# Kernel tuning notes

Measured on AMD Instinct MI355X. Metric: run time of the kernel, lower is better.

The kernel has to match this reference:

```python
import jax, jax.numpy as jnp
import numpy as np

# irreps multiplicities
MUL0_N, MUL1_N = 64, 32   # node:   64x0e + 32x1o  -> dim 160
MUL0_E, MUL1_E = 8, 8     # edge:    8x0e +  8x1o  -> dim 32
MUL0_H, MUL1_H = 64, 32   # hidden: 64x0e + 32x1o  -> dim 160
N_NODES, N_EDGES = 50000, 800000
D_NODE = MUL0_N + 3 * MUL1_N
D_EDGE = MUL0_E + 3 * MUL1_E
D_HID = MUL0_H + 3 * MUL1_H


def _split(x, mul0, mul1):
    # split flat irreps feature into scalars [.., mul0] and vectors [.., mul1, 3]
    s = x[..., :mul0]
    v = x[..., mul0:].reshape(x.shape[0], mul1, 3)
    return s, v


def fctp_messages(x, e, W1, W2, W3, W4):
    """FullyConnectedTensorProduct(node_irreps, edge_irreps -> hidden_irreps), l<=1.
    Paths: (0e,0e->0e), (1o,1o->0e: delta/sqrt3), (0e,1o->1o), (1o,0e->1o)."""
    xs, xv = _split(x, MUL0_N, MUL1_N)   # [E,64], [E,32,3]
    es, ev = _split(e, MUL0_E, MUL1_E)   # [E,8],  [E,8,3]
    inv_sqrt2 = 1.0 / np.sqrt(2.0)       # 2 paths per output irrep
    s1 = jnp.einsum('ea,eb,abc->ec', xs, es, W1) * (1.0 / np.sqrt(MUL0_N * MUL0_E))
    s2 = jnp.einsum('eai,ebi,abc->ec', xv, ev, W2) * (1.0 / (np.sqrt(3.0) * np.sqrt(MUL1_N * MUL1_E)))
    out_s = (s1 + s2) * inv_sqrt2                         # [E,64]
    v1 = jnp.einsum('ea,ebi,abc->eci', xs, ev, W3) * (1.0 / np.sqrt(MUL0_N * MUL1_E))
    v2 = jnp.einsum('eai,eb,abc->eci', xv, es, W4) * (1.0 / np.sqrt(MUL1_N * MUL0_E))
    out_v = (v1 + v2) * inv_sqrt2                         # [E,32,3]
    return jnp.concatenate([out_s, out_v.reshape(out_v.shape[0], -1)], axis=-1)  # [E,160]


def setup_inputs() -> dict:
    key = jax.random.key(0)
    ks = jax.random.split(key, 12)
    node_features = jax.random.normal(ks[0], (N_NODES, D_NODE), dtype=jnp.float32)
    edge_index = jax.random.randint(ks[1], (2, N_EDGES), 0, N_NODES, dtype=jnp.int64)
    edge_attr_tensor = jax.random.normal(ks[2], (N_EDGES, D_EDGE), dtype=jnp.float32)
    node_attr_scalar_raw = jax.random.normal(ks[3], (N_NODES, 1), dtype=jnp.float32)
    # FCTP path weights (mul_in1, mul_in2, mul_out)
    W1 = jax.random.normal(ks[4], (MUL0_N, MUL0_E, MUL0_H), dtype=jnp.float32)
    W2 = jax.random.normal(ks[5], (MUL1_N, MUL1_E, MUL0_H), dtype=jnp.float32)
    W3 = jax.random.normal(ks[6], (MUL0_N, MUL1_E, MUL1_H), dtype=jnp.float32)
    W4 = jax.random.normal(ks[7], (MUL1_N, MUL0_E, MUL1_H), dtype=jnp.float32)
    # runtime-fallback dense layers (Gate raises at runtime in the original)
    Wm = jax.random.normal(ks[8], (D_HID, D_HID), dtype=jnp.float32) / np.sqrt(D_HID)
    bm = jnp.zeros((D_HID,), dtype=jnp.float32)
    Wu = jax.random.normal(ks[9], (D_NODE + D_HID, D_NODE), dtype=jnp.float32) / np.sqrt(D_NODE + D_HID)
    bu = jnp.zeros((D_NODE,), dtype=jnp.float32)
    return {"node_features": node_features, "edge_index": edge_index,
            "edge_attr_tensor": edge_attr_tensor, "node_attr_scalar_raw": node_attr_scalar_raw,
            "W1": W1, "W2": W2, "W3": W3, "W4": W4,
            "Wm": Wm, "bm": bm, "Wu": Wu, "bu": bu}


def reference(node_features, edge_index, edge_attr_tensor, node_attr_scalar_raw,
              W1, W2, W3, W4, Wm, bm, Wu, bu):
    row, col = edge_index[0], edge_index[1]
    # gather source nodes + equivariant tensor-product message
    tp = fctp_messages(node_features[col], edge_attr_tensor, W1, W2, W3, W4)  # [E,160]
    messages = tp @ Wm + bm                                                   # [E,160]
    # scatter-sum aggregation to destination nodes
    agg = jax.ops.segment_sum(messages, row, num_segments=N_NODES)            # [N,160]
    # update (runtime fallback: linear on concat) + residual
    upd = jnp.concatenate([node_features, agg], axis=-1) @ Wu + bu            # [N,160]
    return node_features + upd
```

## Files before the change

kernel.cpp:

```cpp
#include <hip/hip_runtime.h>
#include <hip/hip_bf16.h>

#define NN 50000
#define NE 800000
#define DN 160
#define DE 32
#define NP 50176

typedef __attribute__((ext_vector_type(2))) _Float16 f16x2;
typedef __attribute__((ext_vector_type(8))) _Float16 f16x8;
typedef __attribute__((ext_vector_type(4))) float f32x4;
typedef __attribute__((ext_vector_type(4))) unsigned short u16x4;

#define R2 0.81649658092772603f
#define R4 1.41421356237309515f
#define SC (1.0f/32.0f)

#define XST 172
#define EST 38

union AF { f16x2 p[4]; f16x8 v; };

__device__ __forceinline__ unsigned short f16bits(float f) {
    union { _Float16 h; unsigned short s; } u;
    u.h = (_Float16)f;
    return u.s;
}

__global__ __launch_bounds__(256) void xprep_kernel(const float* __restrict__ x,
                                                    unsigned short* __restrict__ xb) {
    int i = blockIdx.x * 256 + threadIdx.x;
    if (i < NN * DN / 4) {
        const float4 v = reinterpret_cast<const float4*>(x)[i];
        u16x4 p; p[0] = f16bits(v.x); p[1] = f16bits(v.y); p[2] = f16bits(v.z); p[3] = f16bits(v.w);
        reinterpret_cast<u16x4*>(xb)[i] = p;
    }
}

__global__ __launch_bounds__(256) void zero_kernel(float* __restrict__ T,
                                                   int* __restrict__ cnt) {
    int i = blockIdx.x * 256 + threadIdx.x;
    if (i < NN * DN) T[i] = 0.0f;
    if (i < NP) cnt[i] = 0;
}

__global__ __launch_bounds__(256) void hist_kernel(const int* __restrict__ eidx,
                                                   int* __restrict__ cnt) {
    int e = blockIdx.x * 256 + threadIdx.x;
    if (e < NE) atomicAdd(&cnt[eidx[e]], 1);
}

__global__ __launch_bounds__(256) void scan1_kernel(const int* __restrict__ cnt,
                                                    int* __restrict__ cursor,
                                                    int* __restrict__ bsum) {
    __shared__ int s[256];
    const int t = threadIdx.x;
    const int i = blockIdx.x * 256 + t;
    const int v = cnt[i];
    s[t] = v; __syncthreads();
    for (int off = 1; off < 256; off <<= 1) {
        int u = (t >= off) ? s[t - off] : 0;
        __syncthreads(); s[t] += u; __syncthreads();
    }
    cursor[i] = s[t] - v;
    if (t == 255) bsum[blockIdx.x] = s[255];
}

__global__ __launch_bounds__(256) void scan2_kernel(int* __restrict__ bsum) {
    __shared__ int s[256];
    const int t = threadIdx.x;
    const int v = (t < 196) ? bsum[t] : 0;
    s[t] = v; __syncthreads();
    for (int off = 1; off < 256; off <<= 1) {
        int u = (t >= off) ? s[t - off] : 0;
        __syncthreads(); s[t] += u; __syncthreads();
    }
    if (t < 196) bsum[t] = s[t] - v;
}

__global__ __launch_bounds__(256) void scan3_kernel(int* __restrict__ cursor,
                                                    const int* __restrict__ bsum) {
    int i = blockIdx.x * 256 + threadIdx.x;
    cursor[i] += bsum[blockIdx.x];
}

__global__ __launch_bounds__(256) void scatter_kernel(const int* __restrict__ eidx,
                                                      int* __restrict__ cursor,
                                                      int* __restrict__ sorted) {
    int e = blockIdx.x * 256 + threadIdx.x;
    if (e < NE) {
        int pos = atomicAdd(&cursor[eidx[e]], 1);
        sorted[pos] = e;
    }
}

__global__ __launch_bounds__(256) void wprep_edge_kernel(
    const float* __restrict__ W1, const float* __restrict__ W2,
    const float* __restrict__ W3, const float* __restrict__ W4,
    unsigned short* __restrict__ Wh)
{
    int id = blockIdx.x * 256 + threadIdx.x;
    if (id >= 73728) return;
    int j = id & 7, l = (id >> 3) & 63, st = id >> 9;
    int tt = st / 6, s = st % 6;
    int k = 32 * tt + 8 * (l >> 4) + j;
    float w;
    if (s < 4) {
        int c = s * 16 + (l & 15);
        if (k < 512) { int a = k >> 3, b = k & 7; w = W1[(a*8+b)*64 + c] * SC; }
        else { int k2 = k - 512; int a = k2 >> 3, b = k2 & 7; w = W2[(a*8+b)*64 + c] * (R2*SC); }
    } else {
        int c = (s - 4) * 16 + (l & 15);
        if (k < 512) { int a = k >> 3, b = k & 7; w = W3[(a*8+b)*32 + c] * SC; }
        else { int k2 = k - 512; int a = k2 >> 3, b = k2 & 7; w = W4[(a*8+b)*32 + c] * (R4*SC); }
    }
    Wh[id] = f16bits(w);
}

__global__ __launch_bounds__(256) void wcomp_kernel(
    const float* __restrict__ Wm, const float* __restrict__ bm,
    const float* __restrict__ Wu, float* __restrict__ Wc, float* __restrict__ bc)
{
    int id = blockIdx.x * 256 + threadIdx.x;
    if (id < 160 * 160) {
        int k = id / 160, c = id % 160;
        float s = 0.0f;
        for (int h = 0; h < 160; ++h) s = fmaf(Wm[k*160 + h], Wu[(160 + h)*160 + c], s);
        Wc[id] = s;
    }
    if (id < 160) {
        float s = 0.0f;
        for (int h = 0; h < 160; ++h) s = fmaf(bm[h], Wu[(160 + h)*160 + id], s);
        bc[id] = s;
    }
}

__global__ __launch_bounds__(256) void wprep_node_kernel(
    const float* __restrict__ Wu, const float* __restrict__ Wc,
    unsigned short* __restrict__ Wn)
{
    int id = blockIdx.x * 256 + threadIdx.x;
    if (id >= 51200) return;
    int j = id & 7, l = (id >> 3) & 63, tn = id >> 9;
    int tk = tn % 10, n16 = tn / 10;
    int c = n16 * 16 + (l & 15);
    int k = 32 * tk + 8 * (l >> 4) + j;
    float w;
    if (k < 160) {
        w = Wu[k * 160 + c];
    } else {
        int tcol = k - 160;
        int orig = (tcol < 64) ? tcol : 64 + ((tcol - 64) & 31) * 3 + ((tcol - 64) >> 5);
        w = Wc[orig * 160 + c];
    }
    Wn[id] = f16bits(w);
}

__device__ __forceinline__ void makeA(int tt, int g, int er,
    const unsigned short* __restrict__ xls,
    const f16x2 es2[4], const f16x2 ev2[3][4],
    AF& aS, AF& aV0, AF& aV1, AF& aV2)
{
    if (tt < 16) {
        const _Float16 xa = *reinterpret_cast<const _Float16*>(&xls[er*XST + 4*tt + g]);
        const f16x2 xa2 = (f16x2){xa, xa};
        #pragma unroll
        for (int p = 0; p < 4; ++p) {
            aS.p[p]  = xa2 * es2[p];
            aV0.p[p] = xa2 * ev2[0][p];
            aV1.p[p] = xa2 * ev2[1][p];
            aV2.p[p] = xa2 * ev2[2][p];
        }
    } else {
        const int a = 4 * (tt - 16) + g;
        const _Float16 x0 = *reinterpret_cast<const _Float16*>(&xls[er*XST + 64 + a*3 + 0]);
        const _Float16 x1 = *reinterpret_cast<const _Float16*>(&xls[er*XST + 64 + a*3 + 1]);
        const _Float16 x2 = *reinterpret_cast<const _Float16*>(&xls[er*XST + 64 + a*3 + 2]);
        const f16x2 x02 = (f16x2){x0, x0};
        const f16x2 x12 = (f16x2){x1, x1};
        const f16x2 x22 = (f16x2){x2, x2};
        #pragma unroll
        for (int p = 0; p < 4; ++p) {
            f16x2 d = x02 * ev2[0][p];
            d += x12 * ev2[1][p];
            d += x22 * ev2[2][p];
            aS.p[p]  = d;
            aV0.p[p] = x02 * es2[p];
            aV1.p[p] = x12 * es2[p];
            aV2.p[p] = x22 * es2[p];
        }
    }
}

template<int UXB>
__global__ __launch_bounds__(256, 3) void edge_kernel(
    const float* __restrict__ x, const unsigned short* __restrict__ xb,
    const int* __restrict__ eidx, const float* __restrict__ ea,
    const unsigned short* __restrict__ Wh,
    const int* __restrict__ sorted, float* __restrict__ T)
{
    __shared__ __align__(16) char smem[64*XST*2 + 64*EST*2];
    __shared__ int rowls[64];
    __shared__ int colls[64];
    __shared__ int sels[64];

    unsigned short* xls = (unsigned short*)smem;
    unsigned short* els = (unsigned short*)(smem + 64*XST*2);

    const int t = threadIdx.x;
    const int base = blockIdx.x * 64;

    if (t < 64) {
        const int se = sorted[base + t];
        sels[t] = se;
        rowls[t] = eidx[se];
        colls[t] = eidx[NE + se];
    }
    __syncthreads();

    if (UXB) {
        for (int j = t; j < 64 * 40; j += 256) {
            int m = j / 40, q = j - m * 40;
            const u16x4 v = *reinterpret_cast<const u16x4*>(xb + (size_t)colls[m] * DN + q * 4);
            *reinterpret_cast<u16x4*>(&xls[m*XST + q*4]) = v;
        }
    } else {
        for (int j = t; j < 64 * 40; j += 256) {
            int m = j / 40, q = j - m * 40;
            const float4 v = *reinterpret_cast<const float4*>(x + (size_t)colls[m] * DN + q * 4);
            u16x4 p; p[0] = f16bits(v.x); p[1] = f16bits(v.y); p[2] = f16bits(v.z); p[3] = f16bits(v.w);
            *reinterpret_cast<u16x4*>(&xls[m*XST + q*4]) = p;
        }
    }
    for (int j = t; j < 64 * 8; j += 256) {
        int m = j >> 3, q = j & 7;
        const float4 v = *reinterpret_cast<const float4*>(ea + (size_t)sels[m] * DE + q * 4);
        #pragma unroll
        for (int z = 0; z < 4; ++z) {
            int p = q * 4 + z;
            float val = (z == 0) ? v.x : (z == 1) ? v.y : (z == 2) ? v.z : v.w;
            int dst = (p < 8) ? p : 8 + ((p - 8) % 3) * 8 + (p - 8) / 3;
            els[m*EST + dst] = f16bits(val);
        }
    }
    __syncthreads();

    const int lane = t & 63;
    const int wv = t >> 6;
    const int r = lane & 15;
    const int g = lane >> 4;
    const int er = wv * 16 + r;

    f16x2 es2[4], ev2[3][4];
    #pragma unroll
    for (int p = 0; p < 4; ++p) {
        es2[p] = *reinterpret_cast<const f16x2*>(&els[er*EST + 2*p]);
        #pragma unroll
        for (int i = 0; i < 3; ++i)
            ev2[i][p] = *reinterpret_cast<const f16x2*>(&els[er*EST + 8 + i*8 + 2*p]);
    }

    f32x4 accS[4], accV[3][2];
    #pragma unroll
    for (int n = 0; n < 4; ++n) accS[n] = (f32x4){0.f, 0.f, 0.f, 0.f};
    #pragma unroll
    for (int i = 0; i < 3; ++i)
        #pragma unroll
        for (int n = 0; n < 2; ++n) accV[i][n] = (f32x4){0.f, 0.f, 0.f, 0.f};

    const unsigned short* wp = Wh + (size_t)lane * 8;

    f16x8 B0[6], B1[6];
    #pragma unroll
    for (int n = 0; n < 6; ++n)
        B0[n] = *reinterpret_cast<const f16x8*>(wp + n * 512);
    wp += 3072;

#define EDGE_MFMAS(B)                                                             \
    do {                                                                          \
        accS[0] = __builtin_amdgcn_mfma_f32_16x16x32_f16(aS.v,  B[0], accS[0],0,0,0); \
        accS[1] = __builtin_amdgcn_mfma_f32_16x16x32_f16(aS.v,  B[1], accS[1],0,0,0); \
        accS[2] = __builtin_amdgcn_mfma_f32_16x16x32_f16(aS.v,  B[2], accS[2],0,0,0); \
        accS[3] = __builtin_amdgcn_mfma_f32_16x16x32_f16(aS.v,  B[3], accS[3],0,0,0); \
        accV[0][0] = __builtin_amdgcn_mfma_f32_16x16x32_f16(aV0.v, B[4], accV[0][0],0,0,0); \
        accV[0][1] = __builtin_amdgcn_mfma_f32_16x16x32_f16(aV0.v, B[5], accV[0][1],0,0,0); \
        accV[1][0] = __builtin_amdgcn_mfma_f32_16x16x32_f16(aV1.v, B[4], accV[1][0],0,0,0); \
        accV[1][1] = __builtin_amdgcn_mfma_f32_16x16x32_f16(aV1.v, B[5], accV[1][1],0,0,0); \
        accV[2][0] = __builtin_amdgcn_mfma_f32_16x16x32_f16(aV2.v, B[4], accV[2][0],0,0,0); \
        accV[2][1] = __builtin_amdgcn_mfma_f32_16x16x32_f16(aV2.v, B[5], accV[2][1],0,0,0); \
    } while (0)

    for (int tt = 0; tt < 24; tt += 2) {
        #pragma unroll
        for (int n = 0; n < 6; ++n)
            B1[n] = *reinterpret_cast<const f16x8*>(wp + n * 512);
        wp += 3072;

        {
            AF aS, aV0, aV1, aV2;
            makeA(tt, g, er, xls, es2, ev2, aS, aV0, aV1, aV2);
            EDGE_MFMAS(B0);
        }

        if (tt + 2 < 24) {
            #pragma unroll
            for (int n = 0; n < 6; ++n)
                B0[n] = *reinterpret_cast<const f16x8*>(wp + n * 512);
            wp += 3072;
        }

        {
            AF aS, aV0, aV1, aV2;
            makeA(tt + 1, g, er, xls, es2, ev2, aS, aV0, aV1, aV2);
            EDGE_MFMAS(B1);
        }
    }
#undef EDGE_MFMAS

    __syncthreads();
    float* accw = (float*)smem;

    #pragma unroll
    for (int half = 0; half < 2; ++half) {
        if ((wv >> 1) == half) {
            const int lbase = (wv & 1) * 16 + g * 4;
            #pragma unroll
            for (int reg = 0; reg < 4; ++reg) {
                const int lrow = lbase + reg;
                #pragma unroll
                for (int n = 0; n < 4; ++n)
                    accw[lrow*161 + n*16 + r] = accS[n][reg];
                #pragma unroll
                for (int i = 0; i < 3; ++i)
                    #pragma unroll
                    for (int n = 0; n < 2; ++n)
                        accw[lrow*161 + 64 + i*32 + n*16 + r] = accV[i][n][reg];
            }
        }
        __syncthreads();

        if (t < DN) {
            const int col = t;
            const int ebase = half * 32;
            float s = 0.0f;
            int rstart = 0;
            for (int e = 0; e < 32; ++e) {
                s += accw[e*161 + col];
                const int ge = ebase + e;
                if (e == 31 || rowls[ge] != rowls[ge + 1]) {
                    float* dst = T + (size_t)rowls[ge] * DN + col;
                    if (rstart == 0 || e == 31) atomicAdd(dst, s);
                    else *dst = s;
                    s = 0.0f; rstart = e + 1;
                }
            }
        }
        __syncthreads();
    }
}

template<int UXB>
__global__ __launch_bounds__(256) void node_kernel(
    const float* __restrict__ x, const unsigned short* __restrict__ xb,
    float* __restrict__ T, const int* __restrict__ cnt,
    const unsigned short* __restrict__ Wn,
    const float* __restrict__ bu, const float* __restrict__ bc)
{
    __shared__ __align__(16) unsigned short A[64][328];
    const int t = threadIdx.x;
    const int nb = blockIdx.x * 64;

    if (UXB) {
        for (int j = t; j < 64 * 40; j += 256) {
            int m = j / 40, q = j - m * 40;
            int row = nb + m; if (row >= NN) row = NN - 1;
            const u16x4 v = *reinterpret_cast<const u16x4*>(xb + (size_t)row * DN + q * 4);
            *reinterpret_cast<u16x4*>(&A[m][q*4]) = v;
        }
    } else {
        for (int j = t; j < 64 * 40; j += 256) {
            int m = j / 40, q = j - m * 40;
            int row = nb + m; if (row >= NN) row = NN - 1;
            const float4 v = *reinterpret_cast<const float4*>(x + (size_t)row * DN + q * 4);
            u16x4 p; p[0] = f16bits(v.x); p[1] = f16bits(v.y); p[2] = f16bits(v.z); p[3] = f16bits(v.w);
            *reinterpret_cast<u16x4*>(&A[m][q*4]) = p;
        }
    }
    for (int j = t; j < 64 * 40; j += 256) {
        int m = j / 40, q = j - m * 40;
        int row = nb + m; if (row >= NN) row = NN - 1;
        const float4 v = *reinterpret_cast<const float4*>(T + (size_t)row * DN + q * 4);
        u16x4 p; p[0] = f16bits(v.x); p[1] = f16bits(v.y); p[2] = f16bits(v.z); p[3] = f16bits(v.w);
        *reinterpret_cast<u16x4*>(&A[m][160 + q*4]) = p;
    }
    __syncthreads();

    const int lane = t & 63;
    const int wv = t >> 6;
    const int r = lane & 15, g = lane >> 4;
    const int er = wv * 16 + r;

    f32x4 acc[10];
    #pragma unroll
    for (int n = 0; n < 10; ++n) acc[n] = (f32x4){0.f, 0.f, 0.f, 0.f};

    for (int tk = 0; tk < 10; ++tk) {
        const f16x8 a = *reinterpret_cast<const f16x8*>(&A[er][32 * tk + 8 * g]);
        #pragma unroll
        for (int n = 0; n < 10; ++n) {
            const f16x8 b = *reinterpret_cast<const f16x8*>(Wn + ((size_t)(n * 10 + tk) * 64 + lane) * 8);
            acc[n] = __builtin_amdgcn_mfma_f32_16x16x32_f16(a, b, acc[n], 0, 0, 0);
        }
    }

    #pragma unroll
    for (int reg = 0; reg < 4; ++reg) {
        const int nrow = nb + wv * 16 + g * 4 + reg;
        if (nrow < NN) {
            const float dg = (float)cnt[nrow];
            #pragma unroll
            for (int n = 0; n < 10; ++n) {
                const int c = n * 16 + r;
                T[(size_t)nrow * DN + c] =
                    acc[n][reg] + x[(size_t)nrow * DN + c] + bu[c] + dg * bc[c];
            }
        }
    }
}

extern "C" void kernel_launch(void* const* d_in, const int* in_sizes, int n_in,
                              void* d_out, int out_size, void* d_ws, size_t ws_size,
                              hipStream_t stream) {
    const float* xf   = (const float*)d_in[0];
    const int*   eidx = (const int*)d_in[1];
    const float* ea   = (const float*)d_in[2];
    const float* W1 = (const float*)d_in[4];
    const float* W2 = (const float*)d_in[5];
    const float* W3 = (const float*)d_in[6];
    const float* W4 = (const float*)d_in[7];
    const float* Wm = (const float*)d_in[8];
    const float* bm = (const float*)d_in[9];
    const float* Wu = (const float*)d_in[10];
    const float* bu = (const float*)d_in[11];

    float* out = (float*)d_out;

    char* ws = (char*)d_ws;
    int*            cnt    = (int*)ws;
    int*            cursor = (int*)(ws + (256 << 10));
    int*            sorted = (int*)(ws + (512 << 10));
    int*            bsum   = (int*)(ws + (3968 << 10));
    unsigned short* Wh     = (unsigned short*)(ws + (4096 << 10));
    float*          Wc     = (float*)(ws + (4352 << 10));
    float*          bc     = (float*)(ws + (4480 << 10));
    unsigned short* Wn     = (unsigned short*)(ws + (4608 << 10));
    unsigned short* xb     = (unsigned short*)(ws + (4864 << 10));

    const bool uxb = ws_size >= ((size_t)(4864 + 16000) << 10);

    wcomp_kernel<<<100, 256, 0, stream>>>(Wm, bm, Wu, Wc, bc);
    wprep_node_kernel<<<200, 256, 0, stream>>>(Wu, Wc, Wn);
    wprep_edge_kernel<<<288, 256, 0, stream>>>(W1, W2, W3, W4, Wh);
    if (uxb) xprep_kernel<<<(NN * DN / 4 + 255) / 256, 256, 0, stream>>>(xf, xb);
    zero_kernel<<<(NN * DN + 255) / 256, 256, 0, stream>>>(out, cnt);
    hist_kernel<<<NE / 256, 256, 0, stream>>>(eidx, cnt);
    scan1_kernel<<<NP / 256, 256, 0, stream>>>(cnt, cursor, bsum);
    scan2_kernel<<<1, 256, 0, stream>>>(bsum);
    scan3_kernel<<<NP / 256, 256, 0, stream>>>(cursor, bsum);
    scatter_kernel<<<NE / 256, 256, 0, stream>>>(eidx, cursor, sorted);
    if (uxb) {
        edge_kernel<1><<<NE / 64, 256, 0, stream>>>(xf, xb, eidx, ea, Wh, sorted, out);
        node_kernel<1><<<(NN + 63) / 64, 256, 0, stream>>>(xf, xb, out, cnt, Wn, bu, bc);
    } else {
        edge_kernel<0><<<NE / 64, 256, 0, stream>>>(xf, xb, eidx, ea, Wh, sorted, out);
        node_kernel<0><<<(NN + 63) / 64, 256, 0, stream>>>(xf, xb, out, cnt, Wn, bu, bc);
    }
}
```

Before: 517.9 us.

## Stage edge-kernel weight tiles through LDS with async global_load_lds double buffering

Replaces per-wave register double-buffered global loads of the packed weight matrix with a cooperative block-wide copy into a two-slot LDS buffer using global_load_lds. Each of the 24 k-steps then reads its B fragments from LDS, behind a barrier per step. The aim is to cut redundant global/L2 traffic, since every wave used to load the full weight tile itself, and to free registers. In exchange it adds 24 block barriers and extra LDS use (12 KB), which may lower occupancy. It also relies on the async LDS loads completing before the barrier, which only holds if the compiler inserts a vmcnt wait there.

New measurement: 469.5 us. 9.3% less time.

```diff
diff --git a/kernel.cpp b/kernel.cpp
--- a/kernel.cpp
+++ b/kernel.cpp
@@ -25,6 +25,12 @@
     union { _Float16 h; unsigned short s; } u;
     u.h = (_Float16)f;
     return u.s;
+}
+
+__device__ __forceinline__ void load_lds16(const void* g, void* l) {
+    __builtin_amdgcn_global_load_lds(
+        (const __attribute__((address_space(1))) unsigned int*)g,
+        (__attribute__((address_space(3))) unsigned int*)l, 16, 0, 0);
 }
 
 __global__ __launch_bounds__(256) void xprep_kernel(const float* __restrict__ x,
@@ -199,13 +205,14 @@
     const unsigned short* __restrict__ Wh,
     const int* __restrict__ sorted, float* __restrict__ T)
 {
-    __shared__ __align__(16) char smem[64*XST*2 + 64*EST*2];
+    __shared__ __align__(16) char smem[64*XST*2 + 64*EST*2 + 2*3072*2];
     __shared__ int rowls[64];
     __shared__ int colls[64];
     __shared__ int sels[64];
 
-    unsigned short* xls = (unsigned short*)smem;
-    unsigned short* els = (unsigned short*)(smem + 64*XST*2);
+    unsigned short* xls  = (unsigned short*)smem;
+    unsigned short* els  = (unsigned short*)(smem + 64*XST*2);
+    unsigned short* wbuf = (unsigned short*)(smem + 64*XST*2 + 64*EST*2);
 
     const int t = threadIdx.x;
     const int base = blockIdx.x * 64;
@@ -243,7 +250,6 @@
             els[m*EST + dst] = f16bits(val);
         }
     }
-    __syncthreads();
 
     const int lane = t & 63;
     const int wv = t >> 6;
@@ -251,6 +257,19 @@
     const int g = lane >> 4;
     const int er = wv * 16 + r;
 
+    #define STAGE_W(buf, tt)                                                       \
+        do {                                                                       \
+            const unsigned short* wsrc = Wh + (size_t)(tt) * 3072;                 \
+            unsigned short* wdst = wbuf + (buf) * 3072;                            \
+            load_lds16(wsrc + wv * 512 + lane * 8, wdst + wv * 512);               \
+            if (wv < 2)                                                            \
+                load_lds16(wsrc + (wv + 4) * 512 + lane * 8, wdst + (wv + 4) * 512); \
+        } while (0)
+
+    STAGE_W(0, 0);
+
+    __syncthreads();
+
     f16x2 es2[4], ev2[3][4];
     #pragma unroll
     for (int p = 0; p < 4; ++p) {
@@ -268,54 +287,32 @@
         #pragma unroll
         for (int n = 0; n < 2; ++n) accV[i][n] = (f32x4){0.f, 0.f, 0.f, 0.f};
 
-    const unsigned short* wp = Wh + (size_t)lane * 8;
-
-    f16x8 B0[6], B1[6];
-    #pragma unroll
-    for (int n = 0; n < 6; ++n)
-        B0[n] = *reinterpret_cast<const f16x8*>(wp + n * 512);
-    wp += 3072;
-
-#define EDGE_MFMAS(B)                                                             \
-    do {                                                                          \
-        accS[0] = __builtin_amdgcn_mfma_f32_16x16x32_f16(aS.v,  B[0], accS[0],0,0,0); \
-        accS[1] = __builtin_amdgcn_mfma_f32_16x16x32_f16(aS.v,  B[1], accS[1],0,0,0); \
-        accS[2] = __builtin_amdgcn_mfma_f32_16x16x32_f16(aS.v,  B[2], accS[2],0,0,0); \
-        accS[3] = __builtin_amdgcn_mfma_f32_16x16x32_f16(aS.v,  B[3], accS[3],0,0,0); \
-        accV[0][0] = __builtin_amdgcn_mfma_f32_16x16x32_f16(aV0.v, B[4], accV[0][0],0,0,0); \
-        accV[0][1] = __builtin_amdgcn_mfma_f32_16x16x32_f16(aV0.v, B[5], accV[0][1],0,0,0); \
-        accV[1][0] = __builtin_amdgcn_mfma_f32_16x16x32_f16(aV1.v, B[4], accV[1][0],0,0,0); \
-        accV[1][1] = __builtin_amdgcn_mfma_f32_16x16x32_f16(aV1.v, B[5], accV[1][1],0,0,0); \
-        accV[2][0] = __builtin_amdgcn_mfma_f32_16x16x32_f16(aV2.v, B[4], accV[2][0],0,0,0); \
-        accV[2][1] = __builtin_amdgcn_mfma_f32_16x16x32_f16(aV2.v, B[5], accV[2][1],0,0,0); \
-    } while (0)
-
-    for (int tt = 0; tt < 24; tt += 2) {
+    for (int tt = 0; tt < 24; ++tt) {
+        const int cur = tt & 1;
+        if (tt) __syncthreads();
+        if (tt + 1 < 24) STAGE_W(cur ^ 1, tt + 1);
+
+        const unsigned short* wb = wbuf + cur * 3072 + lane * 8;
+        f16x8 B[6];
         #pragma unroll
         for (int n = 0; n < 6; ++n)
-            B1[n] = *reinterpret_cast<const f16x8*>(wp + n * 512);
-        wp += 3072;
-
-        {
-            AF aS, aV0, aV1, aV2;
-            makeA(tt, g, er, xls, es2, ev2, aS, aV0, aV1, aV2);
-            EDGE_MFMAS(B0);
-        }
-
-        if (tt + 2 < 24) {
-            #pragma unroll
-            for (int n = 0; n < 6; ++n)
-                B0[n] = *reinterpret_cast<const f16x8*>(wp + n * 512);
-            wp += 3072;
-        }
-
-        {
-            AF aS, aV0, aV1, aV2;
-            makeA(tt + 1, g, er, xls, es2, ev2, aS, aV0, aV1, aV2);
-            EDGE_MFMAS(B1);
-        }
-    }
-#undef EDGE_MFMAS
+            B[n] = *reinterpret_cast<const f16x8*>(wb + n * 512);
+
+        AF aS, aV0, aV1, aV2;
+        makeA(tt, g, er, xls, es2, ev2, aS, aV0, aV1, aV2);
+
+        accS[0] = __builtin_amdgcn_mfma_f32_16x16x32_f16(aS.v,  B[0], accS[0],0,0,0);
+        accS[1] = __builtin_amdgcn_mfma_f32_16x16x32_f16(aS.v,  B[1], accS[1],0,0,0);
+        accS[2] = __builtin_amdgcn_mfma_f32_16x16x32_f16(aS.v,  B[2], accS[2],0,0,0);
+        accS[3] = __builtin_amdgcn_mfma_f32_16x16x32_f16(aS.v,  B[3], accS[3],0,0,0);
+        accV[0][0] = __builtin_amdgcn_mfma_f32_16x16x32_f16(aV0.v, B[4], accV[0][0],0,0,0);
+        accV[0][1] = __builtin_amdgcn_mfma_f32_16x16x32_f16(aV0.v, B[5], accV[0][1],0,0,0);
+        accV[1][0] = __builtin_amdgcn_mfma_f32_16x16x32_f16(aV1.v, B[4], accV[1][0],0,0,0);
+        accV[1][1] = __builtin_amdgcn_mfma_f32_16x16x32_f16(aV1.v, B[5], accV[1][1],0,0,0);
+        accV[2][0] = __builtin_amdgcn_mfma_f32_16x16x32_f16(aV2.v, B[4], accV[2][0],0,0,0);
+        accV[2][1] = __builtin_amdgcn_mfma_f32_16x16x32_f16(aV2.v, B[5], accV[2][1],0,0,0);
+    }
+    #undef STAGE_W
 
     __syncthreads();
     float* accw = (float*)smem;
```
